# Kernel tuning notes

Hardware: AMD Instinct MI355X
Metric: run time of the kernel (lower is better)

Reference implementation:

```python
import jax, jax.numpy as jnp
import numpy as np

B, IN, D, L = 512, 512, 64, 256
WF = 0.5  # writter_f = 1.0 * w_0


def setup_inputs() -> dict:
    key = jax.random.key(0)
    ks = jax.random.split(key, 12)
    u = lambda i, s: jax.random.uniform(ks[i], s, jnp.float32, -0.05, 0.05)
    return {
        "x": jax.random.normal(ks[0], (B, IN), jnp.float32),
        "memory": u(1, (L, L)),
        "kernel_1": u(2, (IN, 60)), "bias_1": jnp.zeros((1, 60), jnp.float32),
        "kernel_2_0": u(3, (60, 50)), "bias_2_0": jnp.zeros((1, 50), jnp.float32),
        "kernel_3_0": u(4, (60, 50)), "bias_3_0": jnp.zeros((1, 50), jnp.float32),
        "kernel_4_0": u(5, (60, 50)), "bias_4_0": jnp.zeros((1, 50), jnp.float32),
        "kernel_2": u(6, (50, D)), "bias_2": jnp.zeros((1, D), jnp.float32),
        "kernel_3": u(7, (50, D)), "bias_3": jnp.zeros((1, D), jnp.float32),
        "kernel_4": u(8, (50, L)), "bias_4": jnp.zeros((1, L), jnp.float32),
        "kernel_r": u(9, (L, D, L)),
        "kernel_w": u(10, (L, D, L)),
        "w_sig": u(11, (L * L, 1)),
    }


def reference(x, memory, kernel_1, bias_1, kernel_2_0, bias_2_0, kernel_3_0,
              bias_3_0, kernel_4_0, bias_4_0, kernel_2, bias_2, kernel_3,
              bias_3, kernel_4, bias_4, kernel_r, kernel_w, w_sig):
    b = x.shape[0]
    l1 = jax.nn.relu(x @ kernel_1 + bias_1)                                  # (B, 60)
    # write path
    lfw = jax.nn.relu(jax.nn.relu(l1 @ kernel_3_0 + bias_3_0) @ kernel_3 + bias_3)  # (B, D)
    lbw = jnp.tanh(jax.nn.relu(l1 @ kernel_4_0 + bias_4_0) @ kernel_4 + bias_4)     # (B, L)
    lw = jax.nn.softmax(jnp.einsum('bd,jdl->jbl', lfw, kernel_w), axis=-1)   # (L, B, L)
    # wj = memory[j] * lwj * (1 + wf * lbw[j]); note lbw[j] indexes BATCH row j
    w = memory[:, None, :] * lw * (1.0 + WF * lbw[:L, None, :])              # (L, B, L)
    mem_new = w.reshape(L * b, L)                                            # concat over j on axis 0
    # read path (uses only first L rows of the updated memory)
    lf = jax.nn.relu(jax.nn.relu(l1 @ kernel_2_0 + bias_2_0) @ kernel_2 + bias_2)   # (B, D)
    lr = jax.nn.softmax(jnp.einsum('bd,idl->ibl', lf, kernel_r), axis=-1)    # (L, B, L)
    readed = (mem_new[:L][:, None, :] * lr).transpose(1, 0, 2).reshape(b, L * L)
    return jax.nn.sigmoid(readed @ w_sig)                                    # (B, 1)
```

## Files before the change

kernel.cpp:

```cpp
#include <hip/hip_runtime.h>
#include <hip/hip_bf16.h>
#include <math.h>


typedef __attribute__((ext_vector_type(8))) short short8;
typedef __attribute__((ext_vector_type(4))) float f32x4;

static __device__ __forceinline__ unsigned short f2bf(float f) {
    __hip_bfloat16 h = __float2bfloat16(f);
    return *reinterpret_cast<unsigned short*>(&h);
}

__global__ __launch_bounds__(256) void k_front(
    const float* __restrict__ x,
    const float* __restrict__ k1,  const float* __restrict__ b1,
    const float* __restrict__ k20, const float* __restrict__ b20,
    const float* __restrict__ k2,  const float* __restrict__ b2,
    const float* __restrict__ k30, const float* __restrict__ b30,
    const float* __restrict__ k3,  const float* __restrict__ b3,
    const float* __restrict__ k40, const float* __restrict__ b40,
    const float* __restrict__ k4,  const float* __restrict__ b4,
    unsigned short* __restrict__ lf_bf,
    float* __restrict__ lfw,
    float* __restrict__ lbw0) {
    __shared__ float xs[512];
    __shared__ float part[4][64];
    __shared__ float l1s[60];
    __shared__ float hid2[50], hid3[50], hid4[50];
    const int b = blockIdx.x, t = threadIdx.x;
    const int c = t & 63, kq = t >> 6;

    xs[t] = x[b * 512 + t];
    xs[t + 256] = x[b * 512 + 256 + t];
    __syncthreads();

    {
        float a = 0.f;
        if (c < 60) {
            const float* xk = xs + kq * 128;
            const float* kp = k1 + (kq * 128) * 60 + c;
#pragma unroll 8
            for (int k = 0; k < 128; ++k) a += xk[k] * kp[k * 60];
        }
        part[kq][c] = a;
    }
    __syncthreads();
    if (t < 60)
        l1s[t] = fmaxf(b1[t] + part[0][t] + part[1][t] + part[2][t] + part[3][t], 0.f);
    __syncthreads();

    if (t < 50) {
        float a = b20[t];
#pragma unroll
        for (int k = 0; k < 60; ++k) a += l1s[k] * k20[k * 50 + t];
        hid2[t] = fmaxf(a, 0.f);
    } else if (t >= 64 && t < 114 && b < 256) {
        const int j = t - 64;
        float a = b30[j];
#pragma unroll
        for (int k = 0; k < 60; ++k) a += l1s[k] * k30[k * 50 + j];
        hid3[j] = fmaxf(a, 0.f);
    } else if (t >= 128 && t < 178 && b == 0) {
        const int j = t - 128;
        float a = b40[j];
#pragma unroll
        for (int k = 0; k < 60; ++k) a += l1s[k] * k40[k * 50 + j];
        hid4[j] = fmaxf(a, 0.f);
    }
    __syncthreads();

    if (t < 64) {
        float a = b2[t];
#pragma unroll
        for (int k = 0; k < 50; ++k) a += hid2[k] * k2[k * 64 + t];
        lf_bf[b * 64 + t] = f2bf(fmaxf(a, 0.f));
    } else if (t < 128 && b < 256) {
        const int j = t - 64;
        float a = b3[j];
#pragma unroll
        for (int k = 0; k < 50; ++k) a += hid3[k] * k3[k * 64 + j];
        lfw[b * 64 + j] = fmaxf(a, 0.f);
    }
    if (b == 0) {
        __syncthreads();
        float a = b4[t];
#pragma unroll
        for (int k = 0; k < 50; ++k) a += hid4[k] * k4[k * 256 + t];
        lbw0[t] = tanhf(a);
    }
}

__global__ __launch_bounds__(512, 2) void k_mainc(
    const unsigned short* __restrict__ lf,
    const float* __restrict__ kernel_r,
    const float* __restrict__ lfw,
    const float* __restrict__ kw,
    const float* __restrict__ mem,
    const float* __restrict__ lbw0,
    const float* __restrict__ wsig,
    float* __restrict__ partial) {
    __shared__ __align__(16) unsigned short KrT[256 * 64];
    __shared__ float cLDS[256];
    __shared__ float wpart[4];
    const int i = blockIdx.x;
    const int tid = threadIdx.x;
    const int lane = tid & 63;
    const int wv = tid >> 6;

    {
        const int l = tid & 255;
        const int dh = tid >> 8;
        const int rot = ((l >> 3) & 15) * 2;
        const float* src = kernel_r + (size_t)i * 16384 + l;
        char* lds = (char*)KrT;
#pragma unroll
        for (int j = 0; j < 16; ++j) {
            const int d = dh * 32 + ((2 * j + rot) & 31);
            const float f0 = src[(size_t)d * 256];
            const float f1 = src[(size_t)(d + 1) * 256];
            const unsigned int pk =
                (unsigned int)f2bf(f0) | ((unsigned int)f2bf(f1) << 16);
            const int byteoff = ((l * 64 + d) * 2) ^ ((l & 7) << 4);
            *(unsigned int*)(lds + byteoff) = pk;
        }
    }

    float e_c = 0.f;
    if (tid < 256) {
        const int l = tid;
        float s = 0.f;
#pragma unroll 8
        for (int d = 0; d < 64; ++d) s += lfw[i * 64 + d] * kw[d * 256 + l];
        e_c = __expf(s);
        float se = e_c;
#pragma unroll
        for (int off = 1; off < 64; off <<= 1) se += __shfl_xor(se, off, 64);
        if (lane == 0) wpart[wv] = se;
    }
    __syncthreads();
    if (tid < 256) {
        const int l = tid;
        const float tot = wpart[0] + wpart[1] + wpart[2] + wpart[3];
        cLDS[l] = mem[l] * (e_c / tot) * (1.f + 0.5f * lbw0[l]) * wsig[i * 256 + l];
    }
    __syncthreads();

    const int c = lane & 15, g = lane >> 4;

    short8 Bf0[16], Bf1[16];
    {
        const char* lds = (const char*)KrT;
#pragma unroll
        for (int n = 0; n < 16; ++n) {
            const int l = n * 16 + c;
            const int base = l * 128 + g * 16;
            Bf0[n] = *(const short8*)(lds + ((base) ^ ((l & 7) << 4)));
            Bf1[n] = *(const short8*)(lds + ((base + 64) ^ ((l & 7) << 4)));
        }
    }
    float ccv[16];
#pragma unroll
    for (int n = 0; n < 16; ++n) ccv[n] = cLDS[n * 16 + c];

#pragma unroll
    for (int p = 0; p < 4; ++p) {
        const int b0 = wv * 64 + p * 16;
        const short8 a0 = *(const short8*)(lf + (b0 + c) * 64 + g * 8);
        const short8 a1 = *(const short8*)(lf + (b0 + c) * 64 + 32 + g * 8);
        f32x4 acc[16];
#pragma unroll
        for (int n = 0; n < 16; ++n) acc[n] = (f32x4){0.f, 0.f, 0.f, 0.f};
#pragma unroll
        for (int n = 0; n < 16; ++n) {
            acc[n] = __builtin_amdgcn_mfma_f32_16x16x32_bf16(a0, Bf0[n], acc[n], 0, 0, 0);
            acc[n] = __builtin_amdgcn_mfma_f32_16x16x32_bf16(a1, Bf1[n], acc[n], 0, 0, 0);
        }
#pragma unroll
        for (int r = 0; r < 4; ++r) {
            float se = 0.f, sw = 0.f;
#pragma unroll
            for (int n = 0; n < 16; ++n) {
                const float e = __expf(acc[n][r]);
                se += e;
                sw += ccv[n] * e;
            }
#pragma unroll
            for (int off = 1; off < 16; off <<= 1) {
                se += __shfl_xor(se, off, 64);
                sw += __shfl_xor(sw, off, 64);
            }
            if (c == 0) partial[(b0 + g * 4 + r) * 256 + i] = sw / se;
        }
    }
}

__global__ __launch_bounds__(256) void k_out2(const float* __restrict__ partial,
                                              float* __restrict__ out) {
    const int t = threadIdx.x;
    const int rq = t >> 6, lane = t & 63;
#pragma unroll
    for (int p = 0; p < 2; ++p) {
        const int row = blockIdx.x * 8 + p * 4 + rq;
        const f32x4 v = *(const f32x4*)&partial[row * 256 + lane * 4];
        float s = v.x + v.y + v.z + v.w;
#pragma unroll
        for (int off = 1; off < 64; off <<= 1) s += __shfl_xor(s, off, 64);
        if (lane == 0) out[row] = 1.f / (1.f + __expf(-s));
    }
}

extern "C" void kernel_launch(void* const* d_in, const int* in_sizes, int n_in,
                              void* d_out, int out_size, void* d_ws, size_t ws_size,
                              hipStream_t stream) {
    (void)in_sizes; (void)n_in; (void)out_size; (void)ws_size;
    const float* x    = (const float*)d_in[0];
    const float* mem  = (const float*)d_in[1];
    const float* k1   = (const float*)d_in[2];
    const float* b1   = (const float*)d_in[3];
    const float* k20  = (const float*)d_in[4];
    const float* b20  = (const float*)d_in[5];
    const float* k30  = (const float*)d_in[6];
    const float* b30  = (const float*)d_in[7];
    const float* k40  = (const float*)d_in[8];
    const float* b40  = (const float*)d_in[9];
    const float* k2   = (const float*)d_in[10];
    const float* b2   = (const float*)d_in[11];
    const float* k3   = (const float*)d_in[12];
    const float* b3   = (const float*)d_in[13];
    const float* k4   = (const float*)d_in[14];
    const float* b4   = (const float*)d_in[15];
    const float* kr   = (const float*)d_in[16];
    const float* kw   = (const float*)d_in[17];
    const float* wsig = (const float*)d_in[18];
    float* out = (float*)d_out;

    float* ws   = (float*)d_ws;
    float* lfw  = ws;
    float* lbw0 = lfw + 256 * 64;
    float* part = lbw0 + 256;
    unsigned short* lf_bf = (unsigned short*)(part + 131072);

    hipLaunchKernelGGL(k_front, dim3(512), dim3(256), 0, stream, x,
                       k1, b1, k20, b20, k2, b2, k30, b30, k3, b3,
                       k40, b40, k4, b4, lf_bf, lfw, lbw0);
    hipLaunchKernelGGL(k_mainc, dim3(256), dim3(512), 0, stream,
                       lf_bf, kr, lfw, kw, mem, lbw0, wsig, part);
    hipLaunchKernelGGL(k_out2,  dim3(64),  dim3(256), 0, stream, part, out);
}
```

Baseline: 32.67 us.

## Fuse front, main and output kernels into one cooperative kernel with grid syncs

```diff
diff --git a/kernel.cpp b/kernel.cpp
--- a/kernel.cpp
+++ b/kernel.cpp
@@ -1,6 +1,9 @@
 #include <hip/hip_runtime.h>
 #include <hip/hip_bf16.h>
+#include <hip/hip_cooperative_groups.h>
 #include <math.h>
+
+namespace cg = cooperative_groups;
 
 
 typedef __attribute__((ext_vector_type(8))) short short8;
@@ -11,7 +14,7 @@
     return *reinterpret_cast<unsigned short*>(&h);
 }
 
-__global__ __launch_bounds__(256) void k_front(
+__global__ __launch_bounds__(512, 1) void k_fused(
     const float* __restrict__ x,
     const float* __restrict__ k1,  const float* __restrict__ b1,
     const float* __restrict__ k20, const float* __restrict__ b20,
@@ -20,92 +23,28 @@
     const float* __restrict__ k3,  const float* __restrict__ b3,
     const float* __restrict__ k40, const float* __restrict__ b40,
     const float* __restrict__ k4,  const float* __restrict__ b4,
+    const float* __restrict__ kernel_r,
+    const float* __restrict__ kw,
+    const float* __restrict__ mem,
+    const float* __restrict__ wsig,
     unsigned short* __restrict__ lf_bf,
     float* __restrict__ lfw,
-    float* __restrict__ lbw0) {
-    __shared__ float xs[512];
-    __shared__ float part[4][64];
-    __shared__ float l1s[60];
-    __shared__ float hid2[50], hid3[50], hid4[50];
-    const int b = blockIdx.x, t = threadIdx.x;
-    const int c = t & 63, kq = t >> 6;
-
-    xs[t] = x[b * 512 + t];
-    xs[t + 256] = x[b * 512 + 256 + t];
-    __syncthreads();
-
-    {
-        float a = 0.f;
-        if (c < 60) {
-            const float* xk = xs + kq * 128;
-            const float* kp = k1 + (kq * 128) * 60 + c;
-#pragma unroll 8
-            for (int k = 0; k < 128; ++k) a += xk[k] * kp[k * 60];
-        }
-        part[kq][c] = a;
-    }
-    __syncthreads();
-    if (t < 60)
-        l1s[t] = fmaxf(b1[t] + part[0][t] + part[1][t] + part[2][t] + part[3][t], 0.f);
-    __syncthreads();
-
-    if (t < 50) {
-        float a = b20[t];
-#pragma unroll
-        for (int k = 0; k < 60; ++k) a += l1s[k] * k20[k * 50 + t];
-        hid2[t] = fmaxf(a, 0.f);
-    } else if (t >= 64 && t < 114 && b < 256) {
-        const int j = t - 64;
-        float a = b30[j];
-#pragma unroll
-        for (int k = 0; k < 60; ++k) a += l1s[k] * k30[k * 50 + j];
-        hid3[j] = fmaxf(a, 0.f);
-    } else if (t >= 128 && t < 178 && b == 0) {
-        const int j = t - 128;
-        float a = b40[j];
-#pragma unroll
-        for (int k = 0; k < 60; ++k) a += l1s[k] * k40[k * 50 + j];
-        hid4[j] = fmaxf(a, 0.f);
-    }
-    __syncthreads();
-
-    if (t < 64) {
-        float a = b2[t];
-#pragma unroll
-        for (int k = 0; k < 50; ++k) a += hid2[k] * k2[k * 64 + t];
-        lf_bf[b * 64 + t] = f2bf(fmaxf(a, 0.f));
-    } else if (t < 128 && b < 256) {
-        const int j = t - 64;
-        float a = b3[j];
-#pragma unroll
-        for (int k = 0; k < 50; ++k) a += hid3[k] * k3[k * 64 + j];
-        lfw[b * 64 + j] = fmaxf(a, 0.f);
-    }
-    if (b == 0) {
-        __syncthreads();
-        float a = b4[t];
-#pragma unroll
-        for (int k = 0; k < 50; ++k) a += hid4[k] * k4[k * 256 + t];
-        lbw0[t] = tanhf(a);
-    }
-}
-
-__global__ __launch_bounds__(512, 2) void k_mainc(
-    const unsigned short* __restrict__ lf,
-    const float* __restrict__ kernel_r,
-    const float* __restrict__ lfw,
-    const float* __restrict__ kw,
-    const float* __restrict__ mem,
-    const float* __restrict__ lbw0,
-    const float* __restrict__ wsig,
-    float* __restrict__ partial) {
+    float* __restrict__ lbw0,
+    float* __restrict__ partial,
+    float* __restrict__ out) {
     __shared__ __align__(16) unsigned short KrT[256 * 64];
+    __shared__ float xs[2][512];
+    __shared__ float part[2][4][64];
+    __shared__ float l1s[2][60];
+    __shared__ float hid2[2][50], hid3[2][50], hid4[50];
     __shared__ float cLDS[256];
     __shared__ float wpart[4];
+
     const int i = blockIdx.x;
     const int tid = threadIdx.x;
     const int lane = tid & 63;
     const int wv = tid >> 6;
+    cg::grid_group grid = cg::this_grid();
 
     {
         const int l = tid & 255;
@@ -125,6 +64,77 @@
         }
     }
 
+    const int h = tid >> 8;
+    const int tt = tid & 255;
+    const int b = 2 * i + h;
+    const int c = tt & 63, kq = tt >> 6;
+
+    xs[h][tt] = x[b * 512 + tt];
+    xs[h][tt + 256] = x[b * 512 + 256 + tt];
+    __syncthreads();
+
+    {
+        float a0 = 0.f, a1 = 0.f, a2 = 0.f, a3 = 0.f;
+        if (c < 60) {
+            const float* xk = xs[h] + kq * 128;
+            const float* kp = k1 + (kq * 128) * 60 + c;
+#pragma unroll 4
+            for (int k = 0; k < 128; k += 4) {
+                a0 += xk[k + 0] * kp[(k + 0) * 60];
+                a1 += xk[k + 1] * kp[(k + 1) * 60];
+                a2 += xk[k + 2] * kp[(k + 2) * 60];
+                a3 += xk[k + 3] * kp[(k + 3) * 60];
+            }
+        }
+        part[h][kq][c] = (a0 + a1) + (a2 + a3);
+    }
+    __syncthreads();
+    if (tt < 60)
+        l1s[h][tt] = fmaxf(b1[tt] + part[h][0][tt] + part[h][1][tt] +
+                           part[h][2][tt] + part[h][3][tt], 0.f);
+    __syncthreads();
+
+    if (tt < 50) {
+        float a = b20[tt];
+#pragma unroll
+        for (int k = 0; k < 60; ++k) a += l1s[h][k] * k20[k * 50 + tt];
+        hid2[h][tt] = fmaxf(a, 0.f);
+    } else if (tt >= 64 && tt < 114 && b < 256) {
+        const int j = tt - 64;
+        float a = b30[j];
+#pragma unroll
+        for (int k = 0; k < 60; ++k) a += l1s[h][k] * k30[k * 50 + j];
+        hid3[h][j] = fmaxf(a, 0.f);
+    } else if (tt >= 128 && tt < 178 && b == 0) {
+        const int j = tt - 128;
+        float a = b40[j];
+#pragma unroll
+        for (int k = 0; k < 60; ++k) a += l1s[h][k] * k40[k * 50 + j];
+        hid4[j] = fmaxf(a, 0.f);
+    }
+    __syncthreads();
+
+    if (tt < 64) {
+        float a = b2[tt];
+#pragma unroll
+        for (int k = 0; k < 50; ++k) a += hid2[h][k] * k2[k * 64 + tt];
+        lf_bf[b * 64 + tt] = f2bf(fmaxf(a, 0.f));
+    } else if (tt < 128 && b < 256) {
+        const int j = tt - 64;
+        float a = b3[j];
+#pragma unroll
+        for (int k = 0; k < 50; ++k) a += hid3[h][k] * k3[k * 64 + j];
+        lfw[b * 64 + j] = fmaxf(a, 0.f);
+    }
+    if (i == 0 && tid < 256) {
+        float a = b4[tid];
+#pragma unroll
+        for (int k = 0; k < 50; ++k) a += hid4[k] * k4[k * 256 + tid];
+        lbw0[tid] = tanhf(a);
+    }
+
+    grid.sync();
+
     float e_c = 0.f;
     if (tid < 256) {
         const int l = tid;
@@ -145,14 +155,14 @@
     }
     __syncthreads();
 
-    const int c = lane & 15, g = lane >> 4;
+    const int cc16 = lane & 15, g = lane >> 4;
 
     short8 Bf0[16], Bf1[16];
     {
         const char* lds = (const char*)KrT;
 #pragma unroll
         for (int n = 0; n < 16; ++n) {
-            const int l = n * 16 + c;
+            const int l = n * 16 + cc16;
             const int base = l * 128 + g * 16;
             Bf0[n] = *(const short8*)(lds + ((base) ^ ((l & 7) << 4)));
             Bf1[n] = *(const short8*)(lds + ((base + 64) ^ ((l & 7) << 4)));
@@ -160,13 +170,13 @@
     }
     float ccv[16];
 #pragma unroll
-    for (int n = 0; n < 16; ++n) ccv[n] = cLDS[n * 16 + c];
+    for (int n = 0; n < 16; ++n) ccv[n] = cLDS[n * 16 + cc16];
 
 #pragma unroll
     for (int p = 0; p < 4; ++p) {
         const int b0 = wv * 64 + p * 16;
-        const short8 a0 = *(const short8*)(lf + (b0 + c) * 64 + g * 8);
-        const short8 a1 = *(const short8*)(lf + (b0 + c) * 64 + 32 + g * 8);
+        const short8 a0 = *(const short8*)(lf_bf + (b0 + cc16) * 64 + g * 8);
+        const short8 a1 = *(const short8*)(lf_bf + (b0 + cc16) * 64 + 32 + g * 8);
         f32x4 acc[16];
 #pragma unroll
         for (int n = 0; n < 16; ++n) acc[n] = (f32x4){0.f, 0.f, 0.f, 0.f};
@@ -189,18 +199,14 @@
                 se += __shfl_xor(se, off, 64);
                 sw += __shfl_xor(sw, off, 64);
             }
-            if (c == 0) partial[(b0 + g * 4 + r) * 256 + i] = sw / se;
-        }
-    }
-}
-
-__global__ __launch_bounds__(256) void k_out2(const float* __restrict__ partial,
-                                              float* __restrict__ out) {
-    const int t = threadIdx.x;
-    const int rq = t >> 6, lane = t & 63;
-#pragma unroll
-    for (int p = 0; p < 2; ++p) {
-        const int row = blockIdx.x * 8 + p * 4 + rq;
+            if (cc16 == 0) partial[(b0 + g * 4 + r) * 256 + i] = sw / se;
+        }
+    }
+
+    grid.sync();
+
+    if (i < 64) {
+        const int row = i * 8 + (tid >> 6);
         const f32x4 v = *(const f32x4*)&partial[row * 256 + lane * 4];
         float s = v.x + v.y + v.z + v.w;
 #pragma unroll
@@ -240,10 +246,13 @@
     float* part = lbw0 + 256;
     unsigned short* lf_bf = (unsigned short*)(part + 131072);
 
-    hipLaunchKernelGGL(k_front, dim3(512), dim3(256), 0, stream, x,
-                       k1, b1, k20, b20, k2, b2, k30, b30, k3, b3,
-                       k40, b40, k4, b4, lf_bf, lfw, lbw0);
-    hipLaunchKernelGGL(k_mainc, dim3(256), dim3(512), 0, stream,
-                       lf_bf, kr, lfw, kw, mem, lbw0, wsig, part);
-    hipLaunchKernelGGL(k_out2,  dim3(64),  dim3(256), 0, stream, part, out);
+    void* args[] = {
+        (void*)&x,   (void*)&k1,  (void*)&b1,  (void*)&k20, (void*)&b20,
+        (void*)&k2,  (void*)&b2,  (void*)&k30, (void*)&b30, (void*)&k3,
+        (void*)&b3,  (void*)&k40, (void*)&b40, (void*)&k4,  (void*)&b4,
+        (void*)&kr,  (void*)&kw,  (void*)&mem, (void*)&wsig,
+        (void*)&lf_bf, (void*)&lfw, (void*)&lbw0, (void*)&part, (void*)&out,
+    };
+    hipLaunchCooperativeKernel((const void*)k_fused, dim3(256), dim3(512),
+                               args, 0, stream);
 }
```

Result: slower. 89.23 us (+173.1%).
